# Kernel tuning notes

Measured on AMD Instinct MI355X. Metric: run time of the kernel, lower is better.

Reference implementation:

```python
import jax, jax.numpy as jnp
import numpy as np

RES = jnp.array([2.0, 2.0, 2.0], dtype=jnp.float32)  # voxel spacing (mm) for x,y,z step distances


def setup_inputs() -> dict:
    key = jax.random.key(0)
    k1, k2 = jax.random.split(key)
    B, H, D, W = 4, 128, 512, 512
    G, P = 72, 65536
    ct_stack = jax.random.normal(k1, (B, H, D, W), dtype=jnp.float32)
    # coords are (x, y, z) voxel-space floats; clamp ranges in forward are (W-1, D-1, H-1)
    scale = jnp.array([W - 1, D - 1, H - 1], dtype=jnp.float32)
    stacked_indices = jax.random.uniform(k2, (1, G, P, 3), dtype=jnp.float32) * scale
    return {"ct_stack": ct_stack, "stacked_indices": stacked_indices}


def reference(ct_stack, stacked_indices):
    B, H, D, W = ct_stack.shape
    _, G, P, _ = stacked_indices.shape
    c = stacked_indices[0]  # [G,P,3]; identical for every batch element (buffer expand)
    x = jnp.clip(c[..., 0], 0, W - 1)
    y = jnp.clip(c[..., 1], 0, D - 1)
    z = jnp.clip(c[..., 2], 0, H - 1)
    x0 = jnp.floor(x).astype(jnp.int32)
    y0 = jnp.floor(y).astype(jnp.int32)
    z0 = jnp.floor(z).astype(jnp.int32)
    x1 = jnp.clip(x0 + 1, 0, W - 1)
    y1 = jnp.clip(y0 + 1, 0, D - 1)
    z1 = jnp.clip(z0 + 1, 0, H - 1)
    xd = x - x0.astype(x.dtype)
    yd = y - y0.astype(y.dtype)
    zd = z - z0.astype(z.dtype)

    ct_flat = ct_stack.reshape(B, H * D * W)
    lin = lambda zz, yy, xx: (zz * D + yy) * W + xx  # linear index into flattened [H,D,W]
    g = lambda idx: jnp.take(ct_flat, idx, axis=1)   # [B,G,P]

    c000 = g(lin(z0, y0, x0)); c001 = g(lin(z0, y0, x1))
    c010 = g(lin(z0, y1, x0)); c011 = g(lin(z0, y1, x1))
    c100 = g(lin(z1, y0, x0)); c101 = g(lin(z1, y0, x1))
    c110 = g(lin(z1, y1, x0)); c111 = g(lin(z1, y1, x1))

    c00 = c000 * (1 - xd) + c001 * xd
    c01 = c010 * (1 - xd) + c011 * xd
    c10 = c100 * (1 - xd) + c101 * xd
    c11 = c110 * (1 - xd) + c111 * xd
    c0 = c00 * (1 - yd) + c01 * yd
    c1 = c10 * (1 - yd) + c11 * yd
    density = c0 * (1 - zd) + c1 * zd  # [B,G,P]

    # per-angle mean physical step size along the sampled line
    diff = c[:, 1:, :] - c[:, :-1, :]          # [G,P-1,3]
    physical_diff = diff * RES
    step_distances = jnp.sqrt(jnp.sum(physical_diff ** 2, axis=-1))  # [G,P-1]
    step_sizes = jnp.mean(step_distances, axis=-1).reshape(1, G, 1)

    cumsum = jnp.cumsum(density, axis=-1) * step_sizes
    cumsum = cumsum + density * step_sizes * 0.5
    return cumsum.reshape(B * G, P, 1)
```

## Files before the change

kernel.cpp:

```cpp
#include <hip/hip_runtime.h>
#include <math.h>

#define BB 4
#define HH 128
#define DD 512
#define WW 512
#define GG 72
#define PP 65536
#define CHUNK 256
#define NCHUNK (PP / CHUNK)
#define HDW (HH * DD * WW)
#define NBRICK (HDW / 8)

typedef _Float16 half4 __attribute__((ext_vector_type(4)));
typedef _Float16 half8 __attribute__((ext_vector_type(8)));
typedef float f4 __attribute__((ext_vector_type(4)));

__global__ __launch_bounds__(256) void k_transpose(
    const float* __restrict__ ct, _Float16* __restrict__ tv)
{
    const int n2  = blockIdx.x * 256 + threadIdx.x;
    const int bxp = n2 & 127;
    const int by  = (n2 >> 7) & 255;
    const int bz  = n2 >> 15;
    const size_t base = ((size_t)(2 * bz) * DD + 2 * by) * WW + 4 * bxp;

    half8 o00, o01, o02, o03;
    half8 o10, o11, o12, o13;
#pragma unroll
    for (int b = 0; b < BB; ++b) {
        const float* v = ct + (size_t)b * HDW + base;
        const f4 f00 = __builtin_nontemporal_load((const f4*)(v));
        const f4 f01 = __builtin_nontemporal_load((const f4*)(v + WW));
        const f4 f10 = __builtin_nontemporal_load((const f4*)(v + (size_t)DD * WW));
        const f4 f11 = __builtin_nontemporal_load((const f4*)(v + (size_t)DD * WW + WW));
        o00[b] = (_Float16)f00[0]; o00[4 + b] = (_Float16)f00[1];
        o01[b] = (_Float16)f01[0]; o01[4 + b] = (_Float16)f01[1];
        o02[b] = (_Float16)f10[0]; o02[4 + b] = (_Float16)f10[1];
        o03[b] = (_Float16)f11[0]; o03[4 + b] = (_Float16)f11[1];
        o10[b] = (_Float16)f00[2]; o10[4 + b] = (_Float16)f00[3];
        o11[b] = (_Float16)f01[2]; o11[4 + b] = (_Float16)f01[3];
        o12[b] = (_Float16)f10[2]; o12[4 + b] = (_Float16)f10[3];
        o13[b] = (_Float16)f11[2]; o13[4 + b] = (_Float16)f11[3];
    }
    _Float16* dst = tv + (size_t)n2 * 64;
    *(half8*)(dst)      = o00;
    *(half8*)(dst + 8)  = o01;
    *(half8*)(dst + 16) = o02;
    *(half8*)(dst + 24) = o03;
    *(half8*)(dst + 32) = o10;
    *(half8*)(dst + 40) = o11;
    *(half8*)(dst + 48) = o12;
    *(half8*)(dst + 56) = o13;
}

__device__ __forceinline__ int brick_off(int zc, int yc, int xc)
{
    const int brick = ((zc >> 1) << 16) | ((yc >> 1) << 8) | (xc >> 1);
    const int inner = ((zc & 1) << 2) | ((yc & 1) << 1) | (xc & 1);
    return (brick << 5) | (inner << 2);
}

struct PS {
    int i[8];
    float xd, yd, zd;
};

__device__ __forceinline__ PS setup_brick(float cx, float cy, float cz)
{
    const float x = fminf(fmaxf(cx, 0.0f), (float)(WW - 1));
    const float y = fminf(fmaxf(cy, 0.0f), (float)(DD - 1));
    const float z = fminf(fmaxf(cz, 0.0f), (float)(HH - 1));
    const int x0 = (int)floorf(x);
    const int y0 = (int)floorf(y);
    const int z0 = (int)floorf(z);
    const int x1 = min(x0 + 1, WW - 1);
    const int y1 = min(y0 + 1, DD - 1);
    const int z1 = min(z0 + 1, HH - 1);
    PS s;
    s.xd = x - (float)x0;
    s.yd = y - (float)y0;
    s.zd = z - (float)z0;
    s.i[0] = brick_off(z0, y0, x0); s.i[1] = brick_off(z0, y0, x1);
    s.i[2] = brick_off(z0, y1, x0); s.i[3] = brick_off(z0, y1, x1);
    s.i[4] = brick_off(z1, y0, x0); s.i[5] = brick_off(z1, y0, x1);
    s.i[6] = brick_off(z1, y1, x0); s.i[7] = brick_off(z1, y1, x1);
    return s;
}

__device__ __forceinline__ void gather8(
    const _Float16* __restrict__ tv, const PS& s, half4 A[8])
{
#pragma unroll
    for (int k = 0; k < 8; ++k) A[k] = *(const half4*)(tv + (size_t)s.i[k]);
}

__device__ __forceinline__ void lerp_store(
    const half4 A[8], const PS& s, float dens[BB],
    float* __restrict__ density, int g, int p)
{
#pragma unroll
    for (int b = 0; b < BB; ++b) {
        const float c000 = (float)A[0][b], c001 = (float)A[1][b];
        const float c010 = (float)A[2][b], c011 = (float)A[3][b];
        const float c100 = (float)A[4][b], c101 = (float)A[5][b];
        const float c110 = (float)A[6][b], c111 = (float)A[7][b];
        const float c00 = c000 * (1.0f - s.xd) + c001 * s.xd;
        const float c01 = c010 * (1.0f - s.xd) + c011 * s.xd;
        const float c10 = c100 * (1.0f - s.xd) + c101 * s.xd;
        const float c11 = c110 * (1.0f - s.xd) + c111 * s.xd;
        const float c0  = c00 * (1.0f - s.yd) + c01 * s.yd;
        const float c1  = c10 * (1.0f - s.yd) + c11 * s.yd;
        dens[b] = c0 * (1.0f - s.zd) + c1 * s.zd;
        __builtin_nontemporal_store(dens[b],
            density + ((size_t)(b * GG + g)) * PP + p);
    }
}

__global__ __launch_bounds__(256) void k_density_h(
    const _Float16* __restrict__ tv,
    const float* __restrict__ coords,
    float* __restrict__ density,
    float* __restrict__ chunk_sums,
    float* __restrict__ step_accum)
{
    const int cpair = blockIdx.x;
    const int g     = blockIdx.y;
    const int t     = threadIdx.x;
    const int c0    = cpair * 2;
    const int p0    = c0 * CHUNK + t;

    __shared__ float cbuf[(2 * CHUNK + 1) * 3];
    const bool last  = (cpair == NCHUNK / 2 - 1);
    const int  nload = last ? 2 * CHUNK * 3 : (2 * CHUNK + 1) * 3;
    const float* src = coords + ((size_t)g * PP + (size_t)c0 * CHUNK) * 3;
    for (int i = t; i < nload; i += 256)
        cbuf[i] = __builtin_nontemporal_load(src + i);
    __syncthreads();

    const float ax = cbuf[3 * t + 0], ay = cbuf[3 * t + 1], az = cbuf[3 * t + 2];
    const int   u  = t + 256;
    const float bx = cbuf[3 * u + 0], by = cbuf[3 * u + 1], bz = cbuf[3 * u + 2];

    float dist0, dist1 = 0.0f;
    {
        const float dx = cbuf[3 * (t + 1) + 0] - ax;
        const float dy = cbuf[3 * (t + 1) + 1] - ay;
        const float dz = cbuf[3 * (t + 1) + 2] - az;
        dist0 = sqrtf(dx * dx + dy * dy + dz * dz);
    }
    if (!(last && t == CHUNK - 1)) {
        const float dx = cbuf[3 * (u + 1) + 0] - bx;
        const float dy = cbuf[3 * (u + 1) + 1] - by;
        const float dz = cbuf[3 * (u + 1) + 2] - bz;
        dist1 = sqrtf(dx * dx + dy * dy + dz * dz);
    }

    const PS s0 = setup_brick(ax, ay, az);
    const PS s1 = setup_brick(bx, by, bz);

    half4 A0[8], A1[8];
    gather8(tv, s0, A0);
    gather8(tv, s1, A1);

    float dens0[BB], dens1[BB];
    lerp_store(A0, s0, dens0, density, g, p0);
    lerp_store(A1, s1, dens1, density, g, p0 + 256);

    __shared__ float wsum[4][10];
    const int lane = t & 63;
    const int wid  = t >> 6;
    float r[10] = {dens0[0], dens0[1], dens0[2], dens0[3], dist0,
                   dens1[0], dens1[1], dens1[2], dens1[3], dist1};
#pragma unroll
    for (int off = 32; off > 0; off >>= 1) {
#pragma unroll
        for (int j = 0; j < 10; ++j) r[j] += __shfl_xor(r[j], off);
    }
    if (lane == 0) {
#pragma unroll
        for (int j = 0; j < 10; ++j) wsum[wid][j] = r[j];
    }
    __syncthreads();
    if (t == 0) {
        float s[10];
#pragma unroll
        for (int j = 0; j < 10; ++j)
            s[j] = wsum[0][j] + wsum[1][j] + wsum[2][j] + wsum[3][j];
#pragma unroll
        for (int b = 0; b < BB; ++b) {
            chunk_sums[((size_t)(b * GG + g)) * NCHUNK + c0]     = s[b];
            chunk_sums[((size_t)(b * GG + g)) * NCHUNK + c0 + 1] = s[5 + b];
        }
        atomicAdd(&step_accum[g], s[4] + s[9]);
    }
}

__global__ __launch_bounds__(256) void k_density(
    const float* __restrict__ ct,
    const float* __restrict__ coords,
    float* __restrict__ density,
    float* __restrict__ chunk_sums,
    float* __restrict__ step_accum)
{
    const int chunk = blockIdx.x;
    const int g     = blockIdx.y;
    const int t     = threadIdx.x;
    const int p     = chunk * CHUNK + t;

    __shared__ float cbuf[(CHUNK + 1) * 3];
    const int nload = (chunk == NCHUNK - 1) ? CHUNK * 3 : (CHUNK + 1) * 3;
    const float* src = coords + ((size_t)g * PP + (size_t)chunk * CHUNK) * 3;
    for (int i = t; i < nload; i += CHUNK) cbuf[i] = src[i];
    __syncthreads();

    const float cx = cbuf[3 * t + 0];
    const float cy = cbuf[3 * t + 1];
    const float cz = cbuf[3 * t + 2];

    float dist = 0.0f;
    if (p < PP - 1) {
        const int nt = 3 * (t + 1);
        const float dx = cbuf[nt + 0] - cx;
        const float dy = cbuf[nt + 1] - cy;
        const float dz = cbuf[nt + 2] - cz;
        dist = sqrtf(dx * dx + dy * dy + dz * dz);
    }

    const float x = fminf(fmaxf(cx, 0.0f), (float)(WW - 1));
    const float y = fminf(fmaxf(cy, 0.0f), (float)(DD - 1));
    const float z = fminf(fmaxf(cz, 0.0f), (float)(HH - 1));
    const int x0 = (int)floorf(x);
    const int y0 = (int)floorf(y);
    const int z0 = (int)floorf(z);
    const int x1 = min(x0 + 1, WW - 1);
    const int y1 = min(y0 + 1, DD - 1);
    const int z1 = min(z0 + 1, HH - 1);
    const float xd = x - (float)x0, yd = y - (float)y0, zd = z - (float)z0;

    const int b00 = (z0 * DD + y0) * WW;
    const int b01 = (z0 * DD + y1) * WW;
    const int b10 = (z1 * DD + y0) * WW;
    const int b11 = (z1 * DD + y1) * WW;

    float dens[BB];
#pragma unroll
    for (int b = 0; b < BB; ++b) {
        const float* v = ct + (size_t)b * HDW;
        const float c000 = v[b00 + x0], c001 = v[b00 + x1];
        const float c010 = v[b01 + x0], c011 = v[b01 + x1];
        const float c100 = v[b10 + x0], c101 = v[b10 + x1];
        const float c110 = v[b11 + x0], c111 = v[b11 + x1];
        const float c00 = c000 * (1.0f - xd) + c001 * xd;
        const float c01 = c010 * (1.0f - xd) + c011 * xd;
        const float c10 = c100 * (1.0f - xd) + c101 * xd;
        const float c11 = c110 * (1.0f - xd) + c111 * xd;
        const float c0  = c00 * (1.0f - yd) + c01 * yd;
        const float c1  = c10 * (1.0f - yd) + c11 * yd;
        dens[b] = c0 * (1.0f - zd) + c1 * zd;
        density[((size_t)(b * GG + g)) * PP + p] = dens[b];
    }

    __shared__ float wsum[4][5];
    const int lane = t & 63;
    const int wid  = t >> 6;
    float r0 = dens[0], r1 = dens[1], r2 = dens[2], r3 = dens[3], rd = dist;
#pragma unroll
    for (int off = 32; off > 0; off >>= 1) {
        r0 += __shfl_xor(r0, off);
        r1 += __shfl_xor(r1, off);
        r2 += __shfl_xor(r2, off);
        r3 += __shfl_xor(r3, off);
        rd += __shfl_xor(rd, off);
    }
    if (lane == 0) {
        wsum[wid][0] = r0; wsum[wid][1] = r1; wsum[wid][2] = r2;
        wsum[wid][3] = r3; wsum[wid][4] = rd;
    }
    __syncthreads();
    if (t == 0) {
        float s0 = 0, s1 = 0, s2 = 0, s3 = 0, sd = 0;
#pragma unroll
        for (int w = 0; w < 4; ++w) {
            s0 += wsum[w][0]; s1 += wsum[w][1]; s2 += wsum[w][2];
            s3 += wsum[w][3]; sd += wsum[w][4];
        }
        chunk_sums[((size_t)(0 * GG + g)) * NCHUNK + chunk] = s0;
        chunk_sums[((size_t)(1 * GG + g)) * NCHUNK + chunk] = s1;
        chunk_sums[((size_t)(2 * GG + g)) * NCHUNK + chunk] = s2;
        chunk_sums[((size_t)(3 * GG + g)) * NCHUNK + chunk] = s3;
        atomicAdd(&step_accum[g], sd);
    }
}

__global__ __launch_bounds__(256) void k_scan_chunks(float* __restrict__ cs)
{
    const int row = blockIdx.x;
    const int t   = threadIdx.x;
    const int lane = t & 63;
    const int wid  = t >> 6;

    float v = cs[(size_t)row * NCHUNK + t];
    const float own = v;
#pragma unroll
    for (int d = 1; d < 64; d <<= 1) {
        const float n = __shfl_up(v, d);
        if (lane >= d) v += n;
    }
    __shared__ float ws[4];
    if (lane == 63) ws[wid] = v;
    __syncthreads();
    float prefix = 0.0f;
    for (int w = 0; w < wid; ++w) prefix += ws[w];
    cs[(size_t)row * NCHUNK + t] = prefix + v - own;
}

__global__ __launch_bounds__(256) void k_output(
    float* __restrict__ out,
    const float* __restrict__ cs,
    const float* __restrict__ step_accum)
{
    const int chunk = blockIdx.x;
    const int g     = blockIdx.y;
    const int t     = threadIdx.x;
    const int p     = chunk * CHUNK + t;
    const int lane  = t & 63;
    const int wid   = t >> 6;

    const float step = step_accum[g] * (2.0f / (float)(PP - 1));

    float d[BB], v[BB];
#pragma unroll
    for (int b = 0; b < BB; ++b) {
        d[b] = __builtin_nontemporal_load(out + ((size_t)(b * GG + g)) * PP + p);
        v[b] = d[b];
    }

#pragma unroll
    for (int dd = 1; dd < 64; dd <<= 1) {
#pragma unroll
        for (int b = 0; b < BB; ++b) {
            const float n = __shfl_up(v[b], dd);
            if (lane >= dd) v[b] += n;
        }
    }
    __shared__ float ws[4][BB];
    if (lane == 63) {
#pragma unroll
        for (int b = 0; b < BB; ++b) ws[wid][b] = v[b];
    }
    __syncthreads();

#pragma unroll
    for (int b = 0; b < BB; ++b) {
        float prefix = 0.0f;
        for (int w = 0; w < wid; ++w) prefix += ws[w][b];
        const float excl = cs[((size_t)(b * GG + g)) * NCHUNK + chunk];
        const float incl = excl + prefix + v[b];
        __builtin_nontemporal_store(step * (incl + 0.5f * d[b]),
            out + ((size_t)(b * GG + g)) * PP + p);
    }
}

extern "C" void kernel_launch(void* const* d_in, const int* in_sizes, int n_in,
                              void* d_out, int out_size, void* d_ws, size_t ws_size,
                              hipStream_t stream)
{
    const float* ct     = (const float*)d_in[0];
    const float* coords = (const float*)d_in[1];
    float* out = (float*)d_out;

    const size_t volBytes = (size_t)HDW * BB * sizeof(_Float16);
    const size_t csCount  = (size_t)BB * GG * NCHUNK;
    const size_t needed   = volBytes + (csCount + GG) * sizeof(float);

    if (ws_size >= needed) {
        _Float16* tv       = (_Float16*)d_ws;
        float* chunk_sums  = (float*)((char*)d_ws + volBytes);
        float* step_accum  = chunk_sums + csCount;

        (void)hipMemsetAsync(step_accum, 0, GG * sizeof(float), stream);
        k_transpose<<<NBRICK / 2 / 256, 256, 0, stream>>>(ct, tv);
        k_density_h<<<dim3(NCHUNK / 2, GG), 256, 0, stream>>>(tv, coords, out, chunk_sums, step_accum);
        k_scan_chunks<<<BB * GG, 256, 0, stream>>>(chunk_sums);
        k_output<<<dim3(NCHUNK, GG), 256, 0, stream>>>(out, chunk_sums, step_accum);
    } else {
        float* chunk_sums  = (float*)d_ws;
        float* step_accum  = chunk_sums + csCount;

        (void)hipMemsetAsync(step_accum, 0, GG * sizeof(float), stream);
        k_density<<<dim3(NCHUNK, GG), 256, 0, stream>>>(ct, coords, out, chunk_sums, step_accum);
        k_scan_chunks<<<BB * GG, 256, 0, stream>>>(chunk_sums);
        k_output<<<dim3(NCHUNK, GG), 256, 0, stream>>>(out, chunk_sums, step_accum);
    }
}
```

Baseline: 1.006 ms.

## Drop memset and chunk-scan kernel; fold chunk prefix into output kernel

Each density block now covers four chunks instead of two and writes per-block distance partials instead of doing atomicAdd into a zeroed accumulator. The memset and the separate chunk-scan kernel are removed. The output kernel recomputes each chunk's exclusive prefix and the per-angle step sum by reducing the chunk-sum row in every block. This saves two launches and the atomics, at the cost of redundant reads and reductions in every output block and more registers in the density kernel.

```diff
diff --git a/kernel.cpp b/kernel.cpp
--- a/kernel.cpp
+++ b/kernel.cpp
@@ -11,6 +11,8 @@
 #define NCHUNK (PP / CHUNK)
 #define HDW (HH * DD * WW)
 #define NBRICK (HDW / 8)
+#define CPB 4
+#define NPART (NCHUNK / CPB)
 
 typedef _Float16 half4 __attribute__((ext_vector_type(4)));
 typedef _Float16 half8 __attribute__((ext_vector_type(8)));
@@ -122,77 +124,81 @@
     const float* __restrict__ coords,
     float* __restrict__ density,
     float* __restrict__ chunk_sums,
-    float* __restrict__ step_accum)
-{
-    const int cpair = blockIdx.x;
+    float* __restrict__ dist_part)
+{
+    const int cquad = blockIdx.x;
     const int g     = blockIdx.y;
     const int t     = threadIdx.x;
-    const int c0    = cpair * 2;
+    const int c0    = cquad * CPB;
     const int p0    = c0 * CHUNK + t;
 
-    __shared__ float cbuf[(2 * CHUNK + 1) * 3];
-    const bool last  = (cpair == NCHUNK / 2 - 1);
-    const int  nload = last ? 2 * CHUNK * 3 : (2 * CHUNK + 1) * 3;
+    __shared__ float cbuf[(CPB * CHUNK + 1) * 3];
+    const bool last  = (cquad == NPART - 1);
+    const int  nload = last ? CPB * CHUNK * 3 : (CPB * CHUNK + 1) * 3;
     const float* src = coords + ((size_t)g * PP + (size_t)c0 * CHUNK) * 3;
     for (int i = t; i < nload; i += 256)
         cbuf[i] = __builtin_nontemporal_load(src + i);
     __syncthreads();
 
-    const float ax = cbuf[3 * t + 0], ay = cbuf[3 * t + 1], az = cbuf[3 * t + 2];
-    const int   u  = t + 256;
-    const float bx = cbuf[3 * u + 0], by = cbuf[3 * u + 1], bz = cbuf[3 * u + 2];
-
-    float dist0, dist1 = 0.0f;
-    {
-        const float dx = cbuf[3 * (t + 1) + 0] - ax;
-        const float dy = cbuf[3 * (t + 1) + 1] - ay;
-        const float dz = cbuf[3 * (t + 1) + 2] - az;
-        dist0 = sqrtf(dx * dx + dy * dy + dz * dz);
-    }
-    if (!(last && t == CHUNK - 1)) {
-        const float dx = cbuf[3 * (u + 1) + 0] - bx;
-        const float dy = cbuf[3 * (u + 1) + 1] - by;
-        const float dz = cbuf[3 * (u + 1) + 2] - bz;
-        dist1 = sqrtf(dx * dx + dy * dy + dz * dz);
-    }
-
-    const PS s0 = setup_brick(ax, ay, az);
-    const PS s1 = setup_brick(bx, by, bz);
-
-    half4 A0[8], A1[8];
-    gather8(tv, s0, A0);
-    gather8(tv, s1, A1);
-
-    float dens0[BB], dens1[BB];
-    lerp_store(A0, s0, dens0, density, g, p0);
-    lerp_store(A1, s1, dens1, density, g, p0 + 256);
-
-    __shared__ float wsum[4][10];
+    float cx[CPB], cy[CPB], cz[CPB];
+    float dist_tot = 0.0f;
+#pragma unroll
+    for (int j = 0; j < CPB; ++j) {
+        const int q = t + 256 * j;
+        cx[j] = cbuf[3 * q + 0];
+        cy[j] = cbuf[3 * q + 1];
+        cz[j] = cbuf[3 * q + 2];
+        if (!(last && j == CPB - 1 && t == CHUNK - 1)) {
+            const float dx = cbuf[3 * q + 3] - cx[j];
+            const float dy = cbuf[3 * q + 4] - cy[j];
+            const float dz = cbuf[3 * q + 5] - cz[j];
+            dist_tot += sqrtf(dx * dx + dy * dy + dz * dz);
+        }
+    }
+
+    PS s[CPB];
+#pragma unroll
+    for (int j = 0; j < CPB; ++j) s[j] = setup_brick(cx[j], cy[j], cz[j]);
+
+    half4 A[CPB][8];
+#pragma unroll
+    for (int j = 0; j < CPB; ++j) gather8(tv, s[j], A[j]);
+
+    float dens[CPB][BB];
+#pragma unroll
+    for (int j = 0; j < CPB; ++j)
+        lerp_store(A[j], s[j], dens[j], density, g, p0 + 256 * j);
+
+    __shared__ float wsum[4][17];
     const int lane = t & 63;
     const int wid  = t >> 6;
-    float r[10] = {dens0[0], dens0[1], dens0[2], dens0[3], dist0,
-                   dens1[0], dens1[1], dens1[2], dens1[3], dist1};
+    float r[17];
+#pragma unroll
+    for (int j = 0; j < CPB; ++j)
+#pragma unroll
+        for (int b = 0; b < BB; ++b) r[j * BB + b] = dens[j][b];
+    r[16] = dist_tot;
 #pragma unroll
     for (int off = 32; off > 0; off >>= 1) {
 #pragma unroll
-        for (int j = 0; j < 10; ++j) r[j] += __shfl_xor(r[j], off);
+        for (int k = 0; k < 17; ++k) r[k] += __shfl_xor(r[k], off);
     }
     if (lane == 0) {
 #pragma unroll
-        for (int j = 0; j < 10; ++j) wsum[wid][j] = r[j];
+        for (int k = 0; k < 17; ++k) wsum[wid][k] = r[k];
     }
     __syncthreads();
     if (t == 0) {
-        float s[10];
-#pragma unroll
-        for (int j = 0; j < 10; ++j)
-            s[j] = wsum[0][j] + wsum[1][j] + wsum[2][j] + wsum[3][j];
-#pragma unroll
-        for (int b = 0; b < BB; ++b) {
-            chunk_sums[((size_t)(b * GG + g)) * NCHUNK + c0]     = s[b];
-            chunk_sums[((size_t)(b * GG + g)) * NCHUNK + c0 + 1] = s[5 + b];
-        }
-        atomicAdd(&step_accum[g], s[4] + s[9]);
+        float sarr[17];
+#pragma unroll
+        for (int k = 0; k < 17; ++k)
+            sarr[k] = wsum[0][k] + wsum[1][k] + wsum[2][k] + wsum[3][k];
+#pragma unroll
+        for (int j = 0; j < CPB; ++j)
+#pragma unroll
+            for (int b = 0; b < BB; ++b)
+                chunk_sums[((size_t)(b * GG + g)) * NCHUNK + c0 + j] = sarr[j * BB + b];
+        dist_part[g * NPART + cquad] = sarr[16];
     }
 }
 
@@ -201,7 +207,7 @@
     const float* __restrict__ coords,
     float* __restrict__ density,
     float* __restrict__ chunk_sums,
-    float* __restrict__ step_accum)
+    float* __restrict__ dist_part)
 {
     const int chunk = blockIdx.x;
     const int g     = blockIdx.y;
@@ -289,36 +295,15 @@
         chunk_sums[((size_t)(1 * GG + g)) * NCHUNK + chunk] = s1;
         chunk_sums[((size_t)(2 * GG + g)) * NCHUNK + chunk] = s2;
         chunk_sums[((size_t)(3 * GG + g)) * NCHUNK + chunk] = s3;
-        atomicAdd(&step_accum[g], sd);
-    }
-}
-
-__global__ __launch_bounds__(256) void k_scan_chunks(float* __restrict__ cs)
-{
-    const int row = blockIdx.x;
-    const int t   = threadIdx.x;
-    const int lane = t & 63;
-    const int wid  = t >> 6;
-
-    float v = cs[(size_t)row * NCHUNK + t];
-    const float own = v;
-#pragma unroll
-    for (int d = 1; d < 64; d <<= 1) {
-        const float n = __shfl_up(v, d);
-        if (lane >= d) v += n;
-    }
-    __shared__ float ws[4];
-    if (lane == 63) ws[wid] = v;
-    __syncthreads();
-    float prefix = 0.0f;
-    for (int w = 0; w < wid; ++w) prefix += ws[w];
-    cs[(size_t)row * NCHUNK + t] = prefix + v - own;
+        dist_part[g * NCHUNK + chunk] = sd;
+    }
 }
 
 __global__ __launch_bounds__(256) void k_output(
     float* __restrict__ out,
     const float* __restrict__ cs,
-    const float* __restrict__ step_accum)
+    const float* __restrict__ dist_part,
+    int npart)
 {
     const int chunk = blockIdx.x;
     const int g     = blockIdx.y;
@@ -327,7 +312,33 @@
     const int lane  = t & 63;
     const int wid   = t >> 6;
 
-    const float step = step_accum[g] * (2.0f / (float)(PP - 1));
+    __shared__ float exl[4];
+    __shared__ float sdist;
+
+    {
+        const float* row = cs + ((size_t)(wid * GG + g)) * NCHUNK;
+        float v = 0.0f;
+#pragma unroll
+        for (int k = 0; k < 4; ++k) {
+            const int idx = lane + 64 * k;
+            const float x = row[idx];
+            v += (idx < chunk) ? x : 0.0f;
+        }
+#pragma unroll
+        for (int off = 32; off > 0; off >>= 1) v += __shfl_xor(v, off);
+        if (lane == 0) exl[wid] = v;
+    }
+    if (wid == 0) {
+        float dv = 0.0f;
+#pragma unroll
+        for (int k = 0; k < 4; ++k) {
+            const int idx = lane + 64 * k;
+            dv += (idx < npart) ? dist_part[g * npart + idx] : 0.0f;
+        }
+#pragma unroll
+        for (int off = 32; off > 0; off >>= 1) dv += __shfl_xor(dv, off);
+        if (lane == 0) sdist = dv;
+    }
 
     float d[BB], v[BB];
 #pragma unroll
@@ -351,11 +362,12 @@
     }
     __syncthreads();
 
+    const float step = sdist * (2.0f / (float)(PP - 1));
 #pragma unroll
     for (int b = 0; b < BB; ++b) {
         float prefix = 0.0f;
         for (int w = 0; w < wid; ++w) prefix += ws[w][b];
-        const float excl = cs[((size_t)(b * GG + g)) * NCHUNK + chunk];
+        const float excl = exl[b];
         const float incl = excl + prefix + v[b];
         __builtin_nontemporal_store(step * (incl + 0.5f * d[b]),
             out + ((size_t)(b * GG + g)) * PP + p);
@@ -372,25 +384,22 @@
 
     const size_t volBytes = (size_t)HDW * BB * sizeof(_Float16);
     const size_t csCount  = (size_t)BB * GG * NCHUNK;
-    const size_t needed   = volBytes + (csCount + GG) * sizeof(float);
+    const size_t dpCount  = (size_t)GG * NCHUNK;
+    const size_t needed   = volBytes + (csCount + dpCount) * sizeof(float);
 
     if (ws_size >= needed) {
         _Float16* tv       = (_Float16*)d_ws;
         float* chunk_sums  = (float*)((char*)d_ws + volBytes);
-        float* step_accum  = chunk_sums + csCount;
-
-        (void)hipMemsetAsync(step_accum, 0, GG * sizeof(float), stream);
+        float* dist_part   = chunk_sums + csCount;
+
         k_transpose<<<NBRICK / 2 / 256, 256, 0, stream>>>(ct, tv);
-        k_density_h<<<dim3(NCHUNK / 2, GG), 256, 0, stream>>>(tv, coords, out, chunk_sums, step_accum);
-        k_scan_chunks<<<BB * GG, 256, 0, stream>>>(chunk_sums);
-        k_output<<<dim3(NCHUNK, GG), 256, 0, stream>>>(out, chunk_sums, step_accum);
+        k_density_h<<<dim3(NCHUNK / CPB, GG), 256, 0, stream>>>(tv, coords, out, chunk_sums, dist_part);
+        k_output<<<dim3(NCHUNK, GG), 256, 0, stream>>>(out, chunk_sums, dist_part, NPART);
     } else {
         float* chunk_sums  = (float*)d_ws;
-        float* step_accum  = chunk_sums + csCount;
-
-        (void)hipMemsetAsync(step_accum, 0, GG * sizeof(float), stream);
-        k_density<<<dim3(NCHUNK, GG), 256, 0, stream>>>(ct, coords, out, chunk_sums, step_accum);
-        k_scan_chunks<<<BB * GG, 256, 0, stream>>>(chunk_sums);
-        k_output<<<dim3(NCHUNK, GG), 256, 0, stream>>>(out, chunk_sums, step_accum);
-    }
-}
+        float* dist_part   = chunk_sums + csCount;
+
+        k_density<<<dim3(NCHUNK, GG), 256, 0, stream>>>(ct, coords, out, chunk_sums, dist_part);
+        k_output<<<dim3(NCHUNK, GG), 256, 0, stream>>>(out, chunk_sums, dist_part, NCHUNK);
+    }
+}
```

Result: slower. 1.044 ms (+3.7%).
